# Kernel optimization log

Hardware: AMD Instinct MI355X
Metric: run time of the kernel (lower is better)

Reference implementation:

```python
import jax, jax.numpy as jnp
import numpy as np

H = 128        # num_hidden
V = 32000      # vocab_size
CD = 256       # channel_dim
T = 21         # max_seq_len (hardcoded in forward_rl)
NS = 5         # multiple_sample default
SOS, EOS = 1, 2


def setup_inputs() -> dict:
    key = jax.random.key(0)
    ks = jax.random.split(key, 12)
    s = 0.08  # param scale ~ 1/sqrt(H)
    f32 = jnp.float32
    return {
        "input_features": jax.random.normal(ks[0], (1024, CD), f32),
        "embed": (jax.random.normal(ks[1], (V, H), f32) * s),
        "W_fc": jax.random.normal(ks[2], (2 * H, CD), f32) * s,
        "b_fc": jnp.zeros((2 * H,), f32),
        "W_ih": jax.random.normal(ks[3], (4 * H, H), f32) * s,
        "b_ih": jnp.zeros((4 * H,), f32),
        "W_hh": jax.random.normal(ks[4], (4 * H, H), f32) * s,
        "b_hh": jnp.zeros((4 * H,), f32),
        "W1": jax.random.normal(ks[5], (H, H), f32) * s,
        "b1": jnp.zeros((H,), f32),
        "W2": jax.random.normal(ks[6], (V, H), f32) * s,
        "b2": jnp.zeros((V,), f32),
    }


def _decode(input_features, embed, W_fc, b_fc, W_ih, b_ih, W_hh, b_hh, W1, b1, W2, b2):
    # sample_n_times: expand each row NS times along batch
    x = jnp.repeat(input_features, NS, axis=0)           # [B, CD], B = 1024*NS
    B = x.shape[0]
    # init_hidden: from_channel_emb -> split into (h, c)
    hc = x @ W_fc.T + b_fc                               # [B, 2H]
    h0, c0 = hc[:, :H], hc[:, H:]

    it0 = jnp.full((B,), SOS, jnp.int32)
    unf0 = jnp.ones((B,), bool)

    def step(carry, _):
        h, c, it, unfinished = carry
        xt = embed[it]                                   # [B, H]
        gates = xt @ W_ih.T + b_ih + h @ W_hh.T + b_hh   # [B, 4H]
        i, f, g, o = jnp.split(gates, 4, axis=1)         # torch LSTMCell gate order
        c_new = jax.nn.sigmoid(f) * c + jax.nn.sigmoid(i) * jnp.tanh(g)
        h_new = jax.nn.sigmoid(o) * jnp.tanh(c_new)
        # classifier: Linear -> Dropout(eval: identity) -> Linear
        logits = (h_new @ W1.T + b1) @ W2.T + b2         # [B, V]
        logprobs = jax.nn.log_softmax(logits, axis=-1)
        # deterministic sampling surrogate (sample_max path): argmax
        it_new = jnp.argmax(logprobs, axis=1).astype(jnp.int32)
        sample_lp = jnp.take_along_axis(logprobs, it_new[:, None], axis=1)[:, 0]
        mask = unfinished.astype(logprobs.dtype)
        it_new = jnp.where(unfinished, it_new, 0)
        unf_new = unfinished & (it_new != EOS)
        return (h_new, c_new, it_new, unf_new), (it_new, sample_lp, mask)

    _, (seq, lps, masks) = jax.lax.scan(step, (h0, c0, it0, unf0), None, length=T)
    # scan stacks along time: [T, B] -> [B, T]
    return seq.T, lps.T, masks.T


def reference(input_features, embed, W_fc, b_fc, W_ih, b_ih, W_hh, b_hh, W1, b1, W2, b2):
    return _decode(input_features, embed, W_fc, b_fc, W_ih, b_ih, W_hh, b_hh, W1, b1, W2, b2)
```

## Files before the change

kernel.cpp:

```cpp
#include <hip/hip_runtime.h>
#include <math.h>
#include <limits.h>

#define H 128
#define V 32000
#define CD 256
#define T_STEPS 21
#define NS 5
#define SOS 1
#define EOS 2
#define B 1024
#define BFULL 5120
#define NCHUNK 250

typedef _Float16 f16;
typedef f16   half8   __attribute__((ext_vector_type(8)));
typedef float floatx4 __attribute__((ext_vector_type(4)));
typedef unsigned short ushort8v __attribute__((ext_vector_type(8)));

#define AS1 __attribute__((address_space(1)))
#define AS3 __attribute__((address_space(3)))

__device__ __forceinline__ float bf2f(unsigned short u) {
    return __uint_as_float(((unsigned)u) << 16);
}

__device__ __forceinline__ float sig32(float x) {
    float t = (float)exp(-(double)x);
    float r = __fadd_rn(1.0f, t);
    return __fdiv_rn(1.0f, r);
}
__device__ __forceinline__ float tanh32(float x) { return (float)tanh((double)x); }

__device__ __forceinline__ double w2dot(const float* __restrict__ pr,
                                        const void* __restrict__ W2_raw,
                                        int v, bool isf) {
    double acc = 0.0;
    if (isf) {
        const float* wv = (const float*)W2_raw + (long)v * H;
        #pragma unroll 8
        for (int k4 = 0; k4 < H / 4; ++k4) {
            float4 wq = *(const float4*)(wv + k4 * 4);
            float4 pq = *(const float4*)(pr + k4 * 4);
            acc += (double)pq.x * (double)wq.x;
            acc += (double)pq.y * (double)wq.y;
            acc += (double)pq.z * (double)wq.z;
            acc += (double)pq.w * (double)wq.w;
        }
    } else {
        const unsigned short* wv = (const unsigned short*)W2_raw + (long)v * H;
        #pragma unroll 8
        for (int k4 = 0; k4 < H / 4; ++k4) {
            ushort4 u = *(const ushort4*)(wv + k4 * 4);
            float4 pq = *(const float4*)(pr + k4 * 4);
            acc += (double)pq.x * (double)bf2f(u.x);
            acc += (double)pq.y * (double)bf2f(u.y);
            acc += (double)pq.z * (double)bf2f(u.z);
            acc += (double)pq.w * (double)bf2f(u.w);
        }
    }
    return acc;
}

__device__ __forceinline__ float hidot(const float* __restrict__ pr,
                                       const f16* __restrict__ whf,
                                       int cc, int rloc, float b2v) {
    const f16* wp = whf + (long)cc * 16384 + rloc * 8;
    float a = 0.f;
    #pragma unroll
    for (int kkg = 0; kkg < 16; ++kkg) {
        half8 hv = *(const half8*)(wp + kkg * 1024);
        float4 p0 = *(const float4*)(pr + kkg * 8);
        float4 p1 = *(const float4*)(pr + kkg * 8 + 4);
        a = fmaf((float)hv[0], p0.x, a);
        a = fmaf((float)hv[1], p0.y, a);
        a = fmaf((float)hv[2], p0.z, a);
        a = fmaf((float)hv[3], p0.w, a);
        a = fmaf((float)hv[4], p1.x, a);
        a = fmaf((float)hv[5], p1.y, a);
        a = fmaf((float)hv[6], p1.z, a);
        a = fmaf((float)hv[7], p1.w, a);
    }
    return fmaf(a, 0.00390625f, b2v);
}

__global__ void k_detect(const unsigned short* __restrict__ e, int* __restrict__ flag) {
    int i = threadIdx.x;
    unsigned short u = e[2 * i];
    int ex = (u >> 7) & 0xFF;
    bool wild = ((u & 0x7FFF) != 0) && (ex < 0x60 || ex > 0x8F);
    unsigned long long m = __ballot(wild);
    if (i == 0) *flag = (m != 0ull) ? 1 : 0;
}

struct TCArgs {
    const void* src[12];
    float*      dst[12];
    int         n[12];
};
__global__ __launch_bounds__(256) void k_transcode_all(TCArgs tc, const int* __restrict__ flag) {
    int which = blockIdx.y;
    float* d = tc.dst[which];
    if (d == nullptr) return;
    int i = blockIdx.x * 256 + threadIdx.x;
    if (i >= tc.n[which]) return;
    if (*flag) d[i] = ((const float*)tc.src[which])[i];
    else       d[i] = bf2f(((const unsigned short*)tc.src[which])[i]);
}

__global__ __launch_bounds__(256) void k_wtr(
    const float* __restrict__ Wih, const float* __restrict__ Whh,
    const float* __restrict__ W1, float* __restrict__ wihT,
    float* __restrict__ whhT, float* __restrict__ w1T) {
    int e = blockIdx.x * 256 + threadIdx.x;
    if (e < 512 * 128) {
        int col = e >> 7, k = e & 127;
        wihT[(k >> 1) * 1024 + col * 2 + (k & 1)] = Wih[e];
    } else if (e < 2 * 512 * 128) {
        int i = e - 512 * 128;
        int col = i >> 7, k = i & 127;
        whhT[(k >> 1) * 1024 + col * 2 + (k & 1)] = Whh[i];
    } else if (e < 2 * 512 * 128 + 128 * 128) {
        int i = e - 2 * 512 * 128;
        int col = i >> 7, k = i & 127;
        w1T[(k >> 1) * 256 + col * 2 + (k & 1)] = W1[i];
    }
}

__global__ __launch_bounds__(256) void k_wsplit(
    const void* __restrict__ W2_raw, unsigned short* __restrict__ wh,
    unsigned short* __restrict__ wl, float* __restrict__ wn,
    const int* __restrict__ flag) {
    int t = blockIdx.x * 256 + threadIdx.x;
    const bool isf = (*flag != 0);
    int vrow = t >> 4;
    int kkg  = t & 15;
    float v[8];
    if (isf) {
        float4 f0 = ((const float4*)W2_raw)[2 * t];
        float4 f1 = ((const float4*)W2_raw)[2 * t + 1];
        v[0] = f0.x; v[1] = f0.y; v[2] = f0.z; v[3] = f0.w;
        v[4] = f1.x; v[5] = f1.y; v[6] = f1.z; v[7] = f1.w;
    } else {
        ushort8v u = ((const ushort8v*)W2_raw)[t];
        #pragma unroll
        for (int i = 0; i < 8; ++i) v[i] = bf2f(u[i]);
    }
    float s = 0.f;
    half8 hv, lv;
    #pragma unroll
    for (int i = 0; i < 8; ++i) {
        s += v[i] * v[i];
        float ws = v[i] * 256.0f;
        f16 hh = (f16)ws;
        hv[i] = hh;
        lv[i] = (f16)(ws - (float)hh);
    }
    int cb = vrow >> 7, rloc = vrow & 127;
    long dst = (long)cb * 16384 + kkg * 1024 + rloc * 8;
    *(half8*)((f16*)wh + dst) = hv;
    *(half8*)((f16*)wl + dst) = lv;
    #pragma unroll
    for (int off = 1; off < 16; off <<= 1) s += __shfl_xor(s, off, 64);
    if (kkg == 0) wn[vrow] = sqrtf(s);
}

__global__ __launch_bounds__(256) void k_prep(
    const float* __restrict__ wn, float* __restrict__ wmax,
    int* __restrict__ it, int* __restrict__ unf) {
    int tid = threadIdx.x;
    if (blockIdx.x < 4) {
        int i = blockIdx.x * 256 + tid;
        it[i] = SOS; unf[i] = 1;
        return;
    }
    __shared__ float red[4];
    float m = 0.f;
    for (int i = tid; i < V; i += 256) m = fmaxf(m, wn[i]);
    #pragma unroll
    for (int off = 1; off < 64; off <<= 1) m = fmaxf(m, __shfl_xor(m, off, 64));
    if ((tid & 63) == 0) red[tid >> 6] = m;
    __syncthreads();
    if (tid == 0) *wmax = fmaxf(fmaxf(red[0], red[1]), fmaxf(red[2], red[3]));
}

__global__ __launch_bounds__(256) void k_init_hc(
    const float* __restrict__ xf, const float* __restrict__ Wfc,
    const float* __restrict__ bfc, float* __restrict__ h, float* __restrict__ c) {
    __shared__ float xl[CD];
    int r = blockIdx.x;
    int j = threadIdx.x;
    xl[j] = xf[(long)r * CD + j];
    __syncthreads();
    const float4* w4 = (const float4*)(Wfc + (long)j * CD);
    double acc = 0.0;
    for (int k4 = 0; k4 < CD / 4; ++k4) {
        float4 w = w4[k4];
        int k = k4 * 4;
        acc += (double)xl[k]     * (double)w.x;
        acc += (double)xl[k + 1] * (double)w.y;
        acc += (double)xl[k + 2] * (double)w.z;
        acc += (double)xl[k + 3] * (double)w.w;
    }
    float hc = __fadd_rn((float)acc, bfc[j]);
    if (j < H) h[(long)r * H + j] = hc;
    else       c[(long)r * H + (j - H)] = hc;
}

__global__ __launch_bounds__(512) void k_gf(
    const float* __restrict__ cmT, const float* __restrict__ csT,
    const void* __restrict__ W2_raw, const unsigned short* __restrict__ whf_,
    const float* __restrict__ b2, const float* __restrict__ wmax,
    const void* __restrict__ embed_raw, float* __restrict__ h, float* __restrict__ c,
    const float* __restrict__ wihT, const float* __restrict__ whhT,
    const float* __restrict__ bih, const float* __restrict__ bhh,
    const float* __restrict__ w1T, const float* __restrict__ b1,
    float* __restrict__ p32, unsigned short* __restrict__ ph,
    unsigned short* __restrict__ pl,
    int* __restrict__ it, int* __restrict__ unf, float* __restrict__ out,
    int t, const int* __restrict__ flag) {
    __shared__ float As[4][256];
    __shared__ float gsh[4][512];
    __shared__ float hl[4][132];
    const bool isf = (*flag != 0);
    const f16* whf = (const f16*)whf_;
    int tid = threadIdx.x;
    int rb = blockIdx.x * 4;
    int lane = tid & 63, wid = tid >> 6;

    if (t > 0 && wid < 4) {
        int r = rb + wid;
        const float* pr = p32 + (long)r * H;

        float pa = pr[lane], pb = pr[lane + 64];
        float pn2 = pa * pa + pb * pb;
        #pragma unroll
        for (int off = 1; off < 64; off <<= 1) pn2 += __shfl_xor(pn2, off, 64);
        float pn = sqrtf(pn2);
        float wmx = *wmax;
        float eps  = 6.0e-5f * pn * wmx + 3e-5f;
        float epsH = 7.0e-4f * pn * wmx + 2e-5f;

        float marr[4];
        float AM = -__builtin_inff();
        #pragma unroll
        for (int i = 0; i < 4; ++i) {
            int cc = lane + 64 * i;
            marr[i] = (cc < NCHUNK) ? cmT[(long)cc * B + r] : -__builtin_inff();
            AM = fmaxf(AM, marr[i]);
        }
        #pragma unroll
        for (int off = 1; off < 64; off <<= 1) AM = fmaxf(AM, __shfl_xor(AM, off, 64));
        double S = 0.0;
        #pragma unroll
        for (int i = 0; i < 4; ++i) {
            int cc = lane + 64 * i;
            if (cc < NCHUNK) S += (double)csT[(long)cc * B + r];
        }
        #pragma unroll
        for (int off = 1; off < 64; off <<= 1) S += __shfl_xor(S, off, 64);

        float thr = AM - eps - epsH;

        float M = -__builtin_inff();
        #pragma unroll 1
        for (int i = 0; i < 4; ++i) {
            unsigned long long mask = __ballot(marr[i] >= AM - eps);
            while (mask) {
                int bsl = __ffsll(mask) - 1;
                mask &= mask - 1;
                int cc = i * 64 + bsl;
                #pragma unroll 1
                for (int q = 0; q < 2; ++q) {
                    int v = cc * 128 + q * 64 + lane;
                    float lt = hidot(pr, whf, cc, q * 64 + lane, b2[v]);
                    if (lt >= thr) {
                        double acc = w2dot(pr, W2_raw, v, isf);
                        float l = __fadd_rn((float)acc, b2[v]);
                        M = fmaxf(M, l);
                    }
                }
            }
        }
        #pragma unroll
        for (int off = 1; off < 64; off <<= 1) M = fmaxf(M, __shfl_xor(M, off, 64));

        float L = (float)(log(S) - (double)M);
        float negL = __fsub_rn(0.0f, L);

        int best = INT_MAX;
        #pragma unroll 1
        for (int i = 0; i < 4 && best == INT_MAX; ++i) {
            unsigned long long mask = __ballot(marr[i] >= AM - eps);
            while (mask && best == INT_MAX) {
                int bsl = __ffsll(mask) - 1;
                mask &= mask - 1;
                int cc = i * 64 + bsl;
                int hit = INT_MAX;
                #pragma unroll 1
                for (int q = 0; q < 2; ++q) {
                    int v = cc * 128 + q * 64 + lane;
                    float lt = hidot(pr, whf, cc, q * 64 + lane, b2[v]);
                    if (lt >= thr) {
                        double acc = w2dot(pr, W2_raw, v, isf);
                        float l  = __fadd_rn((float)acc, b2[v]);
                        float lp = __fsub_rn(__fsub_rn(l, M), L);
                        if (lp == negL && v < hit) hit = v;
                    }
                }
                #pragma unroll
                for (int off = 1; off < 64; off <<= 1) {
                    int oh = __shfl_xor(hit, off, 64);
                    hit = (oh < hit) ? oh : hit;
                }
                if (hit != INT_MAX) best = hit;
            }
        }
        int bi = (best == INT_MAX) ? 0 : best;

        int unfr = unf[r];
        float lp = negL;
        int itn = unfr ? bi : 0;
        int unfn = (unfr && itn != EOS) ? 1 : 0;
        if (lane == 0) { it[r] = itn; unf[r] = unfn; }
        if (lane < NS) {
            long ro = (long)r * NS + lane;
            int tm1 = t - 1;
            out[ro * T_STEPS + tm1] = (float)itn;
            out[(long)BFULL * T_STEPS + ro * T_STEPS + tm1] = lp;
            out[2L * BFULL * T_STEPS + ro * T_STEPS + tm1] = unfr ? 1.0f : 0.0f;
        }
    }
    __syncthreads();

    {
        int r = tid >> 7, kq = (tid & 127) * 2;
        long row = rb + r;
        int tok = it[row];
        float v0, v1;
        if (kq < H) {
            if (isf) {
                float2 f = *(const float2*)((const float*)embed_raw + (long)tok * H + kq);
                v0 = f.x; v1 = f.y;
            } else {
                ushort2 u = *(const ushort2*)((const unsigned short*)embed_raw + (long)tok * H + kq);
                v0 = bf2f(u.x); v1 = bf2f(u.y);
            }
        } else {
            float2 f = *(const float2*)(h + row * H + (kq - H));
            v0 = f.x; v1 = f.y;
        }
        As[r][kq] = v0; As[r][kq + 1] = v1;
    }
    __syncthreads();

    {
        int cg = tid;
        double acc[4] = {};
        const float2* wi2 = (const float2*)wihT + cg;
        #pragma unroll 8
        for (int kp = 0; kp < 64; ++kp) {
            float2 w = wi2[kp * 512];
            #pragma unroll
            for (int r = 0; r < 4; ++r) {
                float2 a2 = *(const float2*)(&As[r][kp * 2]);
                double s0 = acc[r];
                s0 += (double)a2.x * (double)w.x;
                s0 += (double)a2.y * (double)w.y;
                acc[r] = s0;
            }
        }
        float t1[4];
        float bi = bih[cg];
        #pragma unroll
        for (int r = 0; r < 4; ++r) {
            t1[r] = __fadd_rn((float)acc[r], bi);
            acc[r] = 0.0;
        }
        const float2* wh2 = (const float2*)whhT + cg;
        #pragma unroll 8
        for (int kp = 0; kp < 64; ++kp) {
            float2 w = wh2[kp * 512];
            #pragma unroll
            for (int r = 0; r < 4; ++r) {
                float2 a2 = *(const float2*)(&As[r][128 + kp * 2]);
                double s0 = acc[r];
                s0 += (double)a2.x * (double)w.x;
                s0 += (double)a2.y * (double)w.y;
                acc[r] = s0;
            }
        }
        float bh = bhh[cg];
        #pragma unroll
        for (int r = 0; r < 4; ++r)
            gsh[r][cg] = __fadd_rn(__fadd_rn(t1[r], (float)acc[r]), bh);
    }
    __syncthreads();

    {
        int lr = tid >> 7, j = tid & 127;
        long row = rb + lr;
        float gi = gsh[lr][j], gf = gsh[lr][j + 128], gg = gsh[lr][j + 256], go = gsh[lr][j + 384];
        float cv = c[row * 128 + j];
        float si = sig32(gi);
        float sf = sig32(gf);
        float so = sig32(go);
        float tg = tanh32(gg);
        float cn = __fadd_rn(__fmul_rn(sf, cv), __fmul_rn(si, tg));
        float hn = __fmul_rn(so, tanh32(cn));
        c[row * 128 + j] = cn;
        h[row * 128 + j] = hn;
        hl[lr][j] = hn;
    }
    __syncthreads();

    {
        int j = tid & 127;
        int rr = tid >> 7;
        const float2* w12 = (const float2*)w1T + j;
        double acc = 0.0;
        #pragma unroll 8
        for (int kp = 0; kp < 64; ++kp) {
            float2 w = w12[kp * 128];
            float2 a2 = *(const float2*)(&hl[rr][kp * 2]);
            acc += (double)a2.x * (double)w.x;
            acc += (double)a2.y * (double)w.y;
        }
        long row = rb + rr;
        float pv = __fadd_rn((float)acc, b1[j]);
        p32[row * H + j] = pv;
        float ps = pv * 256.0f;
        f16 hh = (f16)ps;
        f16 ll = (f16)(ps - (float)hh);
        ((f16*)ph)[row * H + j] = hh;
        ((f16*)pl)[row * H + j] = ll;
    }
}

__global__ __launch_bounds__(256, 2) void k_vscan_mfma(
    const unsigned short* __restrict__ ph_, const unsigned short* __restrict__ pl_,
    const unsigned short* __restrict__ whf_, const unsigned short* __restrict__ wlf_,
    const float* __restrict__ b2, float* __restrict__ cmT, float* __restrict__ csT) {
    __shared__ f16 Bsh[16384];
    __shared__ f16 Bsl[16384];
    const f16* ph  = (const f16*)ph_;
    const f16* pl  = (const f16*)pl_;
    int tid  = threadIdx.x;
    int lane = tid & 63, wid = tid >> 6;
    int tx = lane & 15, kg = lane >> 4;

    int bid = blockIdx.x;
    int xcd = bid & 7, rb = (bid >> 3) & 3, hi = bid >> 5;
    int cb = hi * 8 + xcd;
    if (cb >= NCHUNK) return;
    int rbw = rb * 256 + wid * 64;
    int vb  = cb * 128;

    {
        const f16* sh = (const f16*)whf_ + (long)cb * 16384;
        const f16* sl = (const f16*)wlf_ + (long)cb * 16384;
        #pragma unroll
        for (int i = 0; i < 8; ++i) {
            int g = tid + 256 * i;
            __builtin_amdgcn_global_load_lds(
                (const AS1 void*)(const void*)(sh + (long)g * 8),
                (AS3 void*)(void*)(Bsh + g * 8), 16, 0, 0);
            __builtin_amdgcn_global_load_lds(
                (const AS1 void*)(const void*)(sl + (long)g * 8),
                (AS3 void*)(void*)(Bsl + g * 8), 16, 0, 0);
        }
    }
    __syncthreads();

    floatx4 acc[4][8];
    #pragma unroll
    for (int m = 0; m < 4; ++m)
        #pragma unroll
        for (int n = 0; n < 8; ++n)
            acc[m][n] = (floatx4){0.f, 0.f, 0.f, 0.f};

    int aoffs[4];
    #pragma unroll
    for (int m = 0; m < 4; ++m) aoffs[m] = (rbw + m * 16 + tx) * H + kg * 8;

    #pragma unroll
    for (int kk = 0; kk < 4; ++kk) {
        half8 Ah[4], Al[4];
        #pragma unroll
        for (int m = 0; m < 4; ++m) {
            Ah[m] = *(const half8*)(ph + aoffs[m] + kk * 32);
            Al[m] = *(const half8*)(pl + aoffs[m] + kk * 32);
        }
        int bbase = (kk * 4 + kg) * 1024 + tx * 8;
        #pragma unroll
        for (int n = 0; n < 8; ++n) {
            half8 Bh = *(const half8*)(Bsh + bbase + n * 128);
            half8 Bl = *(const half8*)(Bsl + bbase + n * 128);
            #pragma unroll
            for (int m = 0; m < 4; ++m)
                acc[m][n] = __builtin_amdgcn_mfma_f32_16x16x32_f16(Ah[m], Bh, acc[m][n], 0, 0, 0);
            #pragma unroll
            for (int m = 0; m < 4; ++m)
                acc[m][n] = __builtin_amdgcn_mfma_f32_16x16x32_f16(Ah[m], Bl, acc[m][n], 0, 0, 0);
            #pragma unroll
            for (int m = 0; m < 4; ++m)
                acc[m][n] = __builtin_amdgcn_mfma_f32_16x16x32_f16(Al[m], Bh, acc[m][n], 0, 0, 0);
        }
    }

    const float S2 = 1.0f / 65536.0f;
    float bb[8];
    #pragma unroll
    for (int n = 0; n < 8; ++n) bb[n] = b2[vb + n * 16 + tx];
    #pragma unroll
    for (int m = 0; m < 4; ++m) {
        #pragma unroll
        for (int r = 0; r < 4; ++r) {
            float mxr = -__builtin_inff();
            float sr = 0.f;
            #pragma unroll
            for (int n = 0; n < 8; ++n) {
                float l = acc[m][n][r] * S2 + bb[n];
                mxr = fmaxf(mxr, l);
                sr += __expf(l);
            }
            #pragma unroll
            for (int off = 1; off < 16; off <<= 1) {
                mxr = fmaxf(mxr, __shfl_xor(mxr, off, 64));
                sr += __shfl_xor(sr, off, 64);
            }
            if (tx == 0) {
                int row = rbw + m * 16 + kg * 4 + r;
                cmT[(long)cb * B + row] = mxr;
                csT[(long)cb * B + row] = sr;
            }
        }
    }
}

__global__ __launch_bounds__(256) void k_final(
    const float* __restrict__ cmT, const float* __restrict__ csT,
    const float* __restrict__ p32, const void* __restrict__ W2_raw,
    const unsigned short* __restrict__ whf_,
    const float* __restrict__ b2, const float* __restrict__ wmax,
    int* __restrict__ it, int* __restrict__ unf,
    float* __restrict__ out, int t, const int* __restrict__ flag) {
    const bool isf = (*flag != 0);
    const f16* whf = (const f16*)whf_;
    int r = blockIdx.x * 4 + (threadIdx.x >> 6);
    int lane = threadIdx.x & 63;
    const float* pr = p32 + (long)r * H;

    float pa = pr[lane], pb = pr[lane + 64];
    float pn2 = pa * pa + pb * pb;
    #pragma unroll
    for (int off = 1; off < 64; off <<= 1) pn2 += __shfl_xor(pn2, off, 64);
    float pn = sqrtf(pn2);
    float wmx = *wmax;
    float eps  = 6.0e-5f * pn * wmx + 3e-5f;
    float epsH = 7.0e-4f * pn * wmx + 2e-5f;

    float marr[4];
    float AM = -__builtin_inff();
    #pragma unroll
    for (int i = 0; i < 4; ++i) {
        int cc = lane + 64 * i;
        marr[i] = (cc < NCHUNK) ? cmT[(long)cc * B + r] : -__builtin_inff();
        AM = fmaxf(AM, marr[i]);
    }
    #pragma unroll
    for (int off = 1; off < 64; off <<= 1) AM = fmaxf(AM, __shfl_xor(AM, off, 64));
    double S = 0.0;
    #pragma unroll
    for (int i = 0; i < 4; ++i) {
        int cc = lane + 64 * i;
        if (cc < NCHUNK) S += (double)csT[(long)cc * B + r];
    }
    #pragma unroll
    for (int off = 1; off < 64; off <<= 1) S += __shfl_xor(S, off, 64);

    float thr = AM - eps - epsH;

    float M = -__builtin_inff();
    #pragma unroll 1
    for (int i = 0; i < 4; ++i) {
        unsigned long long mask = __ballot(marr[i] >= AM - eps);
        while (mask) {
            int b = __ffsll(mask) - 1;
            mask &= mask - 1;
            int cc = i * 64 + b;
            #pragma unroll 1
            for (int q = 0; q < 2; ++q) {
                int v = cc * 128 + q * 64 + lane;
                float lt = hidot(pr, whf, cc, q * 64 + lane, b2[v]);
                if (lt >= thr) {
                    double acc = w2dot(pr, W2_raw, v, isf);
                    float l = __fadd_rn((float)acc, b2[v]);
                    M = fmaxf(M, l);
                }
            }
        }
    }
    #pragma unroll
    for (int off = 1; off < 64; off <<= 1) M = fmaxf(M, __shfl_xor(M, off, 64));

    float L = (float)(log(S) - (double)M);
    float negL = __fsub_rn(0.0f, L);

    int best = INT_MAX;
    #pragma unroll 1
    for (int i = 0; i < 4 && best == INT_MAX; ++i) {
        unsigned long long mask = __ballot(marr[i] >= AM - eps);
        while (mask && best == INT_MAX) {
            int b = __ffsll(mask) - 1;
            mask &= mask - 1;
            int cc = i * 64 + b;
            int hit = INT_MAX;
            #pragma unroll 1
            for (int q = 0; q < 2; ++q) {
                int v = cc * 128 + q * 64 + lane;
                float lt = hidot(pr, whf, cc, q * 64 + lane, b2[v]);
                if (lt >= thr) {
                    double acc = w2dot(pr, W2_raw, v, isf);
                    float l  = __fadd_rn((float)acc, b2[v]);
                    float lp = __fsub_rn(__fsub_rn(l, M), L);
                    if (lp == negL && v < hit) hit = v;
                }
            }
            #pragma unroll
            for (int off = 1; off < 64; off <<= 1) {
                int oh = __shfl_xor(hit, off, 64);
                hit = (oh < hit) ? oh : hit;
            }
            if (hit != INT_MAX) best = hit;
        }
    }
    int bi = (best == INT_MAX) ? 0 : best;

    int unfr = unf[r];
    float lp = negL;
    int itn = unfr ? bi : 0;
    int unfn = (unfr && itn != EOS) ? 1 : 0;
    if (lane == 0) { it[r] = itn; unf[r] = unfn; }
    if (lane < NS) {
        long ro = (long)r * NS + lane;
        out[ro * T_STEPS + t] = (float)itn;
        out[(long)BFULL * T_STEPS + ro * T_STEPS + t] = lp;
        out[2L * BFULL * T_STEPS + ro * T_STEPS + t] = unfr ? 1.0f : 0.0f;
    }
}

extern "C" void kernel_launch(void* const* d_in, const int* in_sizes, int n_in,
                              void* d_out, int out_size, void* d_ws, size_t ws_size,
                              hipStream_t stream) {
    float* out = (float*)d_out;

    char* w = (char*)d_ws;
    float* fin[12];
    for (int i = 0; i < 12; ++i) {
        if (i == 1 || i == 10) { fin[i] = nullptr; continue; }
        fin[i] = (float*)w;
        size_t bytes = ((size_t)in_sizes[i] * 4 + 15) & ~(size_t)15;
        w += bytes;
    }
    float*  h     = (float*) w; w += (size_t)B * H * 4;
    float*  c     = (float*) w; w += (size_t)B * H * 4;
    float*  p32   = (float*) w; w += (size_t)B * H * 4;
    float*  cm    = (float*) w; w += (size_t)B * NCHUNK * 4;
    float*  cs    = (float*) w; w += (size_t)B * NCHUNK * 4;
    float*  wn    = (float*) w; w += (size_t)V * 4;
    float*  wmax  = (float*) w; w += 16;
    int*    it    = (int*)   w; w += (size_t)B * 4;
    int*    unf   = (int*)   w; w += (size_t)B * 4;
    int*    flag  = (int*)   w; w += 16;
    float*  wihT  = (float*) w; w += (size_t)512 * 128 * 4;
    float*  whhT  = (float*) w; w += (size_t)512 * 128 * 4;
    float*  w1T   = (float*) w; w += (size_t)128 * 128 * 4;
    unsigned short* ph = (unsigned short*)w; w += (size_t)B * H * 2;
    unsigned short* pl = (unsigned short*)w; w += (size_t)B * H * 2;
    unsigned short* wh = (unsigned short*)w; w += (size_t)V * H * 2;
    unsigned short* wl = (unsigned short*)w; w += (size_t)V * H * 2;

    k_detect<<<1, 64, 0, stream>>>((const unsigned short*)d_in[1], flag);

    TCArgs tc;
    int maxn = 0;
    for (int i = 0; i < 12; ++i) {
        tc.src[i] = d_in[i];
        tc.dst[i] = fin[i];
        tc.n[i]   = in_sizes[i];
        if (fin[i] && in_sizes[i] > maxn) maxn = in_sizes[i];
    }
    k_transcode_all<<<dim3((maxn + 255) / 256, 12), 256, 0, stream>>>(tc, flag);

    k_wsplit<<<(V * H / 8 + 255) / 256, 256, 0, stream>>>(d_in[10], wh, wl, wn, flag);
    k_wtr<<<(2 * 512 * 128 + 128 * 128 + 255) / 256, 256, 0, stream>>>(
        fin[4], fin[6], fin[8], wihT, whhT, w1T);
    k_prep<<<5, 256, 0, stream>>>(wn, wmax, it, unf);

    const float* xf  = fin[0];
    const float* Wfc = fin[2];
    const float* bfc = fin[3];
    const float* bih = fin[5];
    const float* bhh = fin[7];
    const float* b1  = fin[9];
    const float* b2  = fin[11];

    k_init_hc<<<B, 256, 0, stream>>>(xf, Wfc, bfc, h, c);

    for (int t = 0; t < T_STEPS; ++t) {
        k_gf<<<B / 4, 512, 0, stream>>>(cm, cs, d_in[10], wh, b2, wmax,
                                        d_in[1], h, c, wihT, whhT, bih, bhh,
                                        w1T, b1, p32, ph, pl, it, unf, out, t, flag);
        k_vscan_mfma<<<1024, 256, 0, stream>>>(ph, pl, wh, wl, b2, cm, cs);
    }
    k_final<<<B / 4, 256, 0, stream>>>(cm, cs, p32, d_in[10], wh, b2, wmax, it, unf, out,
                                       T_STEPS - 1, flag);
}
```

Before: 1.657 ms.

## Emit per-chunk candidate bitmasks from vocab scan instead of recomputing fp16 dots

The vocab-scan MFMA kernel now compares each logit against a per-row threshold (chunk max minus an eps built from a precomputed hidden-vector norm) and writes two 64-bit candidate bitmasks per chunk and row. The argmax refinement in k_gf and k_final reads these masks instead of recomputing an fp16 dot over every vocab entry in a surviving chunk before the exact fp64 check. The row norm is computed once in k_gf and stored, so the consumers no longer reduce it themselves. The cost is an extra 4 MB mask buffer written every step and ballot work in the scan epilogue. The filter threshold also changes, from the global max minus two eps terms to the chunk-local max minus one eps, which could in principle drop a true candidate.

```diff
diff --git a/kernel.cpp b/kernel.cpp
--- a/kernel.cpp
+++ b/kernel.cpp
@@ -60,28 +60,6 @@
         }
     }
     return acc;
-}
-
-__device__ __forceinline__ float hidot(const float* __restrict__ pr,
-                                       const f16* __restrict__ whf,
-                                       int cc, int rloc, float b2v) {
-    const f16* wp = whf + (long)cc * 16384 + rloc * 8;
-    float a = 0.f;
-    #pragma unroll
-    for (int kkg = 0; kkg < 16; ++kkg) {
-        half8 hv = *(const half8*)(wp + kkg * 1024);
-        float4 p0 = *(const float4*)(pr + kkg * 8);
-        float4 p1 = *(const float4*)(pr + kkg * 8 + 4);
-        a = fmaf((float)hv[0], p0.x, a);
-        a = fmaf((float)hv[1], p0.y, a);
-        a = fmaf((float)hv[2], p0.z, a);
-        a = fmaf((float)hv[3], p0.w, a);
-        a = fmaf((float)hv[4], p1.x, a);
-        a = fmaf((float)hv[5], p1.y, a);
-        a = fmaf((float)hv[6], p1.z, a);
-        a = fmaf((float)hv[7], p1.w, a);
-    }
-    return fmaf(a, 0.00390625f, b2v);
 }
 
 __global__ void k_detect(const unsigned short* __restrict__ e, int* __restrict__ flag) {
@@ -209,21 +187,22 @@
 
 __global__ __launch_bounds__(512) void k_gf(
     const float* __restrict__ cmT, const float* __restrict__ csT,
-    const void* __restrict__ W2_raw, const unsigned short* __restrict__ whf_,
+    const unsigned long long* __restrict__ maskbuf,
+    const void* __restrict__ W2_raw,
     const float* __restrict__ b2, const float* __restrict__ wmax,
     const void* __restrict__ embed_raw, float* __restrict__ h, float* __restrict__ c,
     const float* __restrict__ wihT, const float* __restrict__ whhT,
     const float* __restrict__ bih, const float* __restrict__ bhh,
     const float* __restrict__ w1T, const float* __restrict__ b1,
     float* __restrict__ p32, unsigned short* __restrict__ ph,
-    unsigned short* __restrict__ pl,
+    unsigned short* __restrict__ pl, float* __restrict__ pnorm,
     int* __restrict__ it, int* __restrict__ unf, float* __restrict__ out,
     int t, const int* __restrict__ flag) {
     __shared__ float As[4][256];
     __shared__ float gsh[4][512];
     __shared__ float hl[4][132];
+    __shared__ float redp[8];
     const bool isf = (*flag != 0);
-    const f16* whf = (const f16*)whf_;
     int tid = threadIdx.x;
     int rb = blockIdx.x * 4;
     int lane = tid & 63, wid = tid >> 6;
@@ -231,15 +210,8 @@
     if (t > 0 && wid < 4) {
         int r = rb + wid;
         const float* pr = p32 + (long)r * H;
-
-        float pa = pr[lane], pb = pr[lane + 64];
-        float pn2 = pa * pa + pb * pb;
-        #pragma unroll
-        for (int off = 1; off < 64; off <<= 1) pn2 += __shfl_xor(pn2, off, 64);
-        float pn = sqrtf(pn2);
         float wmx = *wmax;
-        float eps  = 6.0e-5f * pn * wmx + 3e-5f;
-        float epsH = 7.0e-4f * pn * wmx + 2e-5f;
+        float eps = 6.0e-5f * pnorm[r] * wmx + 3e-5f;
 
         float marr[4];
         float AM = -__builtin_inff();
@@ -259,8 +231,6 @@
         }
         #pragma unroll
         for (int off = 1; off < 64; off <<= 1) S += __shfl_xor(S, off, 64);
-
-        float thr = AM - eps - epsH;
 
         float M = -__builtin_inff();
         #pragma unroll 1
@@ -270,11 +240,11 @@
                 int bsl = __ffsll(mask) - 1;
                 mask &= mask - 1;
                 int cc = i * 64 + bsl;
+                const unsigned long long* mk2 = maskbuf + ((long)cc * B + r) * 2;
                 #pragma unroll 1
                 for (int q = 0; q < 2; ++q) {
-                    int v = cc * 128 + q * 64 + lane;
-                    float lt = hidot(pr, whf, cc, q * 64 + lane, b2[v]);
-                    if (lt >= thr) {
+                    if ((mk2[q] >> lane) & 1ull) {
+                        int v = cc * 128 + q * 64 + lane;
                         double acc = w2dot(pr, W2_raw, v, isf);
                         float l = __fadd_rn((float)acc, b2[v]);
                         M = fmaxf(M, l);
@@ -296,12 +266,12 @@
                 int bsl = __ffsll(mask) - 1;
                 mask &= mask - 1;
                 int cc = i * 64 + bsl;
+                const unsigned long long* mk2 = maskbuf + ((long)cc * B + r) * 2;
                 int hit = INT_MAX;
                 #pragma unroll 1
                 for (int q = 0; q < 2; ++q) {
-                    int v = cc * 128 + q * 64 + lane;
-                    float lt = hidot(pr, whf, cc, q * 64 + lane, b2[v]);
-                    if (lt >= thr) {
+                    if ((mk2[q] >> lane) & 1ull) {
+                        int v = cc * 128 + q * 64 + lane;
                         double acc = w2dot(pr, W2_raw, v, isf);
                         float l  = __fadd_rn((float)acc, b2[v]);
                         float lp = __fsub_rn(__fsub_rn(l, M), L);
@@ -434,13 +404,22 @@
         f16 ll = (f16)(ps - (float)hh);
         ((f16*)ph)[row * H + j] = hh;
         ((f16*)pl)[row * H + j] = ll;
-    }
+        float sq = pv * pv;
+        #pragma unroll
+        for (int off = 1; off < 64; off <<= 1) sq += __shfl_xor(sq, off, 64);
+        if (lane == 0) redp[wid] = sq;
+    }
+    __syncthreads();
+    if (tid < 4) pnorm[rb + tid] = sqrtf(redp[2 * tid] + redp[2 * tid + 1]);
 }
 
 __global__ __launch_bounds__(256, 2) void k_vscan_mfma(
     const unsigned short* __restrict__ ph_, const unsigned short* __restrict__ pl_,
     const unsigned short* __restrict__ whf_, const unsigned short* __restrict__ wlf_,
-    const float* __restrict__ b2, float* __restrict__ cmT, float* __restrict__ csT) {
+    const float* __restrict__ b2, const float* __restrict__ pnorm,
+    const float* __restrict__ wmax,
+    float* __restrict__ cmT, float* __restrict__ csT,
+    unsigned long long* __restrict__ maskbuf) {
     __shared__ f16 Bsh[16384];
     __shared__ f16 Bsl[16384];
     const f16* ph  = (const f16*)ph_;
@@ -509,6 +488,7 @@
     }
 
     const float S2 = 1.0f / 65536.0f;
+    const float wmx = *wmax;
     float bb[8];
     #pragma unroll
     for (int n = 0; n < 8; ++n) bb[n] = b2[vb + n * 16 + tx];
@@ -516,23 +496,35 @@
     for (int m = 0; m < 4; ++m) {
         #pragma unroll
         for (int r = 0; r < 4; ++r) {
+            float l[8];
             float mxr = -__builtin_inff();
             float sr = 0.f;
             #pragma unroll
             for (int n = 0; n < 8; ++n) {
-                float l = acc[m][n][r] * S2 + bb[n];
-                mxr = fmaxf(mxr, l);
-                sr += __expf(l);
+                l[n] = acc[m][n][r] * S2 + bb[n];
+                mxr = fmaxf(mxr, l[n]);
+                sr += __expf(l[n]);
             }
             #pragma unroll
             for (int off = 1; off < 16; off <<= 1) {
                 mxr = fmaxf(mxr, __shfl_xor(mxr, off, 64));
                 sr += __shfl_xor(sr, off, 64);
             }
+            int row = rbw + m * 16 + kg * 4 + r;
+            float thr = mxr - (6.0e-5f * pnorm[row] * wmx + 3.0e-5f);
+            unsigned long long w0 = 0, w1 = 0;
+            #pragma unroll
+            for (int n = 0; n < 8; ++n) {
+                unsigned long long bal = __ballot(l[n] >= thr);
+                unsigned long long piece = (bal >> (kg * 16)) & 0xFFFFull;
+                if (n < 4) w0 |= piece << (n * 16);
+                else       w1 |= piece << ((n - 4) * 16);
+            }
             if (tx == 0) {
-                int row = rbw + m * 16 + kg * 4 + r;
                 cmT[(long)cb * B + row] = mxr;
                 csT[(long)cb * B + row] = sr;
+                maskbuf[((long)cb * B + row) * 2]     = w0;
+                maskbuf[((long)cb * B + row) * 2 + 1] = w1;
             }
         }
     }
@@ -540,25 +532,18 @@
 
 __global__ __launch_bounds__(256) void k_final(
     const float* __restrict__ cmT, const float* __restrict__ csT,
+    const unsigned long long* __restrict__ maskbuf,
     const float* __restrict__ p32, const void* __restrict__ W2_raw,
-    const unsigned short* __restrict__ whf_,
     const float* __restrict__ b2, const float* __restrict__ wmax,
+    const float* __restrict__ pnorm,
     int* __restrict__ it, int* __restrict__ unf,
     float* __restrict__ out, int t, const int* __restrict__ flag) {
     const bool isf = (*flag != 0);
-    const f16* whf = (const f16*)whf_;
     int r = blockIdx.x * 4 + (threadIdx.x >> 6);
     int lane = threadIdx.x & 63;
     const float* pr = p32 + (long)r * H;
-
-    float pa = pr[lane], pb = pr[lane + 64];
-    float pn2 = pa * pa + pb * pb;
-    #pragma unroll
-    for (int off = 1; off < 64; off <<= 1) pn2 += __shfl_xor(pn2, off, 64);
-    float pn = sqrtf(pn2);
     float wmx = *wmax;
-    float eps  = 6.0e-5f * pn * wmx + 3e-5f;
-    float epsH = 7.0e-4f * pn * wmx + 2e-5f;
+    float eps = 6.0e-5f * pnorm[r] * wmx + 3e-5f;
 
     float marr[4];
     float AM = -__builtin_inff();
@@ -578,8 +563,6 @@
     }
     #pragma unroll
     for (int off = 1; off < 64; off <<= 1) S += __shfl_xor(S, off, 64);
-
-    float thr = AM - eps - epsH;
 
     float M = -__builtin_inff();
     #pragma unroll 1
@@ -589,11 +572,11 @@
             int b = __ffsll(mask) - 1;
             mask &= mask - 1;
             int cc = i * 64 + b;
+            const unsigned long long* mk2 = maskbuf + ((long)cc * B + r) * 2;
             #pragma unroll 1
             for (int q = 0; q < 2; ++q) {
-                int v = cc * 128 + q * 64 + lane;
-                float lt = hidot(pr, whf, cc, q * 64 + lane, b2[v]);
-                if (lt >= thr) {
+                if ((mk2[q] >> lane) & 1ull) {
+                    int v = cc * 128 + q * 64 + lane;
                     double acc = w2dot(pr, W2_raw, v, isf);
                     float l = __fadd_rn((float)acc, b2[v]);
                     M = fmaxf(M, l);
@@ -615,12 +598,12 @@
             int b = __ffsll(mask) - 1;
             mask &= mask - 1;
             int cc = i * 64 + b;
+            const unsigned long long* mk2 = maskbuf + ((long)cc * B + r) * 2;
             int hit = INT_MAX;
             #pragma unroll 1
             for (int q = 0; q < 2; ++q) {
-                int v = cc * 128 + q * 64 + lane;
-                float lt = hidot(pr, whf, cc, q * 64 + lane, b2[v]);
-                if (lt >= thr) {
+                if ((mk2[q] >> lane) & 1ull) {
+                    int v = cc * 128 + q * 64 + lane;
                     double acc = w2dot(pr, W2_raw, v, isf);
                     float l  = __fadd_rn((float)acc, b2[v]);
                     float lp = __fsub_rn(__fsub_rn(l, M), L);
@@ -670,12 +653,14 @@
     float*  cs    = (float*) w; w += (size_t)B * NCHUNK * 4;
     float*  wn    = (float*) w; w += (size_t)V * 4;
     float*  wmax  = (float*) w; w += 16;
+    float*  pnorm = (float*) w; w += (size_t)B * 4;
     int*    it    = (int*)   w; w += (size_t)B * 4;
     int*    unf   = (int*)   w; w += (size_t)B * 4;
     int*    flag  = (int*)   w; w += 16;
     float*  wihT  = (float*) w; w += (size_t)512 * 128 * 4;
     float*  whhT  = (float*) w; w += (size_t)512 * 128 * 4;
     float*  w1T   = (float*) w; w += (size_t)128 * 128 * 4;
+    unsigned long long* maskbuf = (unsigned long long*)w; w += (size_t)NCHUNK * B * 16;
     unsigned short* ph = (unsigned short*)w; w += (size_t)B * H * 2;
     unsigned short* pl = (unsigned short*)w; w += (size_t)B * H * 2;
     unsigned short* wh = (unsigned short*)w; w += (size_t)V * H * 2;
@@ -709,11 +694,11 @@
     k_init_hc<<<B, 256, 0, stream>>>(xf, Wfc, bfc, h, c);
 
     for (int t = 0; t < T_STEPS; ++t) {
-        k_gf<<<B / 4, 512, 0, stream>>>(cm, cs, d_in[10], wh, b2, wmax,
+        k_gf<<<B / 4, 512, 0, stream>>>(cm, cs, maskbuf, d_in[10], b2, wmax,
                                         d_in[1], h, c, wihT, whhT, bih, bhh,
-                                        w1T, b1, p32, ph, pl, it, unf, out, t, flag);
-        k_vscan_mfma<<<1024, 256, 0, stream>>>(ph, pl, wh, wl, b2, cm, cs);
-    }
-    k_final<<<B / 4, 256, 0, stream>>>(cm, cs, p32, d_in[10], wh, b2, wmax, it, unf, out,
-                                       T_STEPS - 1, flag);
-}
+                                        w1T, b1, p32, ph, pl, pnorm, it, unf, out, t, flag);
+        k_vscan_mfma<<<1024, 256, 0, stream>>>(ph, pl, wh, wl, b2, pnorm, wmax, cm, cs, maskbuf);
+    }
+    k_final<<<B / 4, 256, 0, stream>>>(cm, cs, maskbuf, p32, d_in[10], b2, wmax, pnorm,
+                                       it, unf, out, T_STEPS - 1, flag);
+}
```

After: 1.776 ms. +7.2%, slower.
